# Optimization experiments

Measured on AMD Instinct MI355X. Metric: run time of the kernel, lower is better.

## Reference

```python
import jax, jax.numpy as jnp
import numpy as np
import math

B, N, D, K, H = 64, 16384, 64, 8, 128
ITERS = 3
LN_EPS = 1e-5  # torch LayerNorm default


def _ln(x, w, b):
    m = jnp.mean(x, axis=-1, keepdims=True)
    v = jnp.mean((x - m) ** 2, axis=-1, keepdims=True)
    return (x - m) * jax.lax.rsqrt(v + LN_EPS) * w + b


def setup_inputs() -> dict:
    key = jax.random.key(0)
    ks = jax.random.split(key, 20)
    s = 1.0 / math.sqrt(D)
    inp = {
        "inputs": jax.random.normal(ks[0], (B, N, D), jnp.float32),
        "noise": jax.random.normal(ks[1], (B, K, D), jnp.float32),
        "slots_mu": jax.random.normal(ks[2], (1, 1, D), jnp.float32),
        "slots_sigma": jax.random.uniform(ks[3], (1, 1, D), jnp.float32, -s, s),
        "ln_in_w": jnp.ones((D,), jnp.float32), "ln_in_b": jnp.zeros((D,), jnp.float32),
        "ln_slots_w": jnp.ones((D,), jnp.float32), "ln_slots_b": jnp.zeros((D,), jnp.float32),
        "ln_ff_w": jnp.ones((D,), jnp.float32), "ln_ff_b": jnp.zeros((D,), jnp.float32),
        "wk": jax.random.uniform(ks[4], (D, D), jnp.float32, -s, s),
        "bk": jax.random.uniform(ks[5], (D,), jnp.float32, -s, s),
        "wq": jax.random.uniform(ks[6], (D, D), jnp.float32, -s, s),
        "bq": jax.random.uniform(ks[7], (D,), jnp.float32, -s, s),
        "wv": jax.random.uniform(ks[8], (D, D), jnp.float32, -s, s),
        "bv": jax.random.uniform(ks[9], (D,), jnp.float32, -s, s),
        "gru_wih": jax.random.uniform(ks[10], (D, 3 * D), jnp.float32, -s, s),
        "gru_bih": jax.random.uniform(ks[11], (3 * D,), jnp.float32, -s, s),
        "gru_whh": jax.random.uniform(ks[12], (D, 3 * D), jnp.float32, -s, s),
        "gru_bhh": jax.random.uniform(ks[13], (3 * D,), jnp.float32, -s, s),
        "mlp_w1": jax.random.uniform(ks[14], (D, H), jnp.float32, -s, s),
        "mlp_b1": jax.random.uniform(ks[15], (H,), jnp.float32, -s, s),
        "mlp_w2": jax.random.uniform(ks[16], (H, D), jnp.float32, -1.0 / math.sqrt(H), 1.0 / math.sqrt(H)),
        "mlp_b2": jax.random.uniform(ks[17], (D,), jnp.float32, -1.0 / math.sqrt(H), 1.0 / math.sqrt(H)),
    }
    return inp


def reference(inputs, noise, slots_mu, slots_sigma, ln_in_w, ln_in_b,
              ln_slots_w, ln_slots_b, ln_ff_w, ln_ff_b,
              wk, bk, wq, bq, wv, bv,
              gru_wih, gru_bih, gru_whh, gru_bhh,
              mlp_w1, mlp_b1, mlp_w2, mlp_b2):
    x = _ln(inputs, ln_in_w, ln_in_b)              # [B, N, D]
    # k, v depend only on (fixed) inputs; original recomputes them each iter
    # with identical values, so hoist for efficiency (same math).
    k = x @ wk + bk                                 # [B, N, D]
    v = x @ wv + bv                                 # [B, N, D]
    slots = slots_mu + slots_sigma * noise          # [B, K, D]
    scale = 1.0 / math.sqrt(D)
    for _ in range(ITERS):
        prev = slots
        q = _ln(slots, ln_slots_w, ln_slots_b) @ wq + bq          # [B, K, D]
        logits = jnp.einsum('bkd,bnd->bkn', q, k) * scale          # [B, K, N]
        attn = jax.nn.softmax(logits, axis=1)  # softmax over slots
        updates = jnp.einsum('bkn,bnd->bkd', attn, v)              # [B, K, D]
        # torch GRUCell: gates ordered (r, z, n)
        gi = updates @ gru_wih + gru_bih                           # [B, K, 3D]
        gh = prev @ gru_whh + gru_bhh
        i_r, i_z, i_n = jnp.split(gi, 3, axis=-1)
        h_r, h_z, h_n = jnp.split(gh, 3, axis=-1)
        r = jax.nn.sigmoid(i_r + h_r)
        z = jax.nn.sigmoid(i_z + h_z)
        n = jnp.tanh(i_n + r * h_n)
        slots = (1.0 - z) * n + z * prev
        h = _ln(slots, ln_ff_w, ln_ff_b)
        slots = slots + (jax.nn.relu(h @ mlp_w1 + mlp_b1) @ mlp_w2 + mlp_b2)
    return slots
```

## Files before the change

kernel.cpp:

```cpp
#include <hip/hip_runtime.h>
#include <math.h>

#define B_ 64
#define N_ 16384
#define D_ 64
#define K_ 8
#define SCALE 0.125f
#define LN_EPS 1e-5f
#define CHUNKS 16
#define ROWS_PER_CHUNK (N_ / CHUNKS)
#define NT 256
#define TILES (ROWS_PER_CHUNK / NT)
#define REC 528

__device__ __forceinline__ float wsum64(float v) {
#pragma unroll
  for (int m = 1; m < 64; m <<= 1) v += __shfl_xor(v, m);
  return v;
}

__global__ void init_slots(const float* __restrict__ noise, const float* __restrict__ mu,
                           const float* __restrict__ sg, float* __restrict__ slots) {
  int i = blockIdx.x * blockDim.x + threadIdx.x;
  int d = i & 63;
  slots[i] = mu[d] + sg[d] * noise[i];
}

__global__ __launch_bounds__(64) void prep_q(
    const float* __restrict__ slots,
    const float* __restrict__ lnsw, const float* __restrict__ lnsb,
    const float* __restrict__ wq, const float* __restrict__ bq,
    const float* __restrict__ wk, const float* __restrict__ bk,
    const float* __restrict__ lniw, const float* __restrict__ lnib,
    float* __restrict__ qprep) {
  const int bk_i = blockIdx.x;
  const int b = bk_i >> 3, kk = bk_i & 7;
  const int d = threadIdx.x;
  __shared__ float xs[64], qsh[64], wkl[64 * 65];
  for (int i = 0; i < 64; ++i) wkl[i * 65 + d] = wk[i * 64 + d];
  float s = slots[bk_i * 64 + d];
  float m = wsum64(s) * (1.f / 64.f);
  float df = s - m;
  float var = wsum64(df * df) * (1.f / 64.f);
  float r = 1.f / sqrtf(var + LN_EPS);
  xs[d] = df * r * lnsw[d] + lnsb[d];
  __syncthreads();
  float q = bq[d];
  for (int c = 0; c < 64; ++c) q += xs[c] * wq[c * 64 + d];
  qsh[d] = q;
  __syncthreads();
  float qp = 0.f, c0 = 0.f;
  for (int dd = 0; dd < 64; ++dd) {
    float qd = qsh[dd];
    qp += wkl[d * 65 + dd] * qd;
    c0 += qd * bk[dd];
  }
  float qw = qp * lniw[d] * SCALE;
  float As = wsum64(qw);
  float Bp = wsum64(qp * lnib[d]);
  float Bc = (Bp + c0) * SCALE;
  float* rec = qprep + b * REC;
  rec[d * 8 + kk] = qw;
  if (d == 0) { rec[512 + kk] = As; rec[520 + kk] = Bc; }
}

__global__ __launch_bounds__(256) void attn_pass(
    const float* __restrict__ inp, const float* __restrict__ qprep,
    float* __restrict__ part) {
  __shared__ float xT[64 * 129];
  __shared__ float awr[4 * 512];
  __shared__ float qwT[512];
  __shared__ float AsBc[16];
  __shared__ float redS[4 * 16];
  __shared__ float accST[16];
  const int tid = threadIdx.x;
  const int b = blockIdx.x >> 4, chunk = blockIdx.x & 15;
  for (int i = tid; i < 512; i += 256) qwT[i] = qprep[b * REC + i];
  if (tid < 16) { AsBc[tid] = qprep[b * REC + 512 + tid]; accST[tid] = 0.f; }
  __syncthreads();
  const int kk0 = (tid >> 6) * 2;
  const int dd = tid & 63;
  float Y0 = 0.f, Y1 = 0.f;
  const float* srcbase = inp + ((size_t)b * N_ + (size_t)chunk * ROWS_PER_CHUNK) * D_;
  for (int t = 0; t < TILES; ++t) {
    const float* src = srcbase + (size_t)(t * NT + tid) * D_;
    float4 x[16];
#pragma unroll
    for (int j = 0; j < 16; ++j) x[j] = reinterpret_cast<const float4*>(src)[j];
    float sum = 0.f, sq = 0.f;
    float l[8];
#pragma unroll
    for (int kk = 0; kk < 8; ++kk) l[kk] = 0.f;
#pragma unroll
    for (int j = 0; j < 16; ++j) {
      float xc[4] = {x[j].x, x[j].y, x[j].z, x[j].w};
#pragma unroll
      for (int e = 0; e < 4; ++e) {
        const int c = j * 4 + e;
        const float v = xc[e];
        sum += v; sq += v * v;
        const float4 qa = *reinterpret_cast<const float4*>(&qwT[c * 8]);
        const float4 qb = *reinterpret_cast<const float4*>(&qwT[c * 8 + 4]);
        l[0] += qa.x * v; l[1] += qa.y * v; l[2] += qa.z * v; l[3] += qa.w * v;
        l[4] += qb.x * v; l[5] += qb.y * v; l[6] += qb.z * v; l[7] += qb.w * v;
      }
    }
    const float m = sum * (1.f / 64.f);
    const float var = sq * (1.f / 64.f) - m * m;
    const float r = 1.f / sqrtf(var + LN_EPS);
    const float mr = m * r;
    float lmax = -1e30f;
#pragma unroll
    for (int kk = 0; kk < 8; ++kk) {
      l[kk] = r * l[kk] - mr * AsBc[kk] + AsBc[8 + kk];
      lmax = fmaxf(lmax, l[kk]);
    }
    float es = 0.f;
#pragma unroll
    for (int kk = 0; kk < 8; ++kk) { l[kk] = expf(l[kk] - lmax); es += l[kk]; }
    const float inv = 1.f / es;
#pragma unroll
    for (int kk = 0; kk < 8; ++kk) l[kk] *= inv;
#pragma unroll
    for (int p = 0; p < 4; ++p) {
      float2 w2; w2.x = l[2 * p] * r; w2.y = l[2 * p + 1] * r;
      *reinterpret_cast<float2*>(&awr[p * 512 + tid * 2]) = w2;
    }
    float red[16];
#pragma unroll
    for (int kk = 0; kk < 8; ++kk) {
      red[kk] = wsum64(l[kk]);
      red[8 + kk] = wsum64(l[kk] * mr);
    }
    if ((tid & 63) == 0) {
      const int w = tid >> 6;
#pragma unroll
      for (int i = 0; i < 16; ++i) redS[w * 16 + i] = red[i];
    }
    __syncthreads();
    if (tid < 16) accST[tid] += redS[tid] + redS[16 + tid] + redS[32 + tid] + redS[48 + tid];
    if (tid < 128) {
#pragma unroll
      for (int j = 0; j < 16; ++j) {
        xT[(j * 4 + 0) * 129 + tid] = x[j].x;
        xT[(j * 4 + 1) * 129 + tid] = x[j].y;
        xT[(j * 4 + 2) * 129 + tid] = x[j].z;
        xT[(j * 4 + 3) * 129 + tid] = x[j].w;
      }
    }
    __syncthreads();
#pragma unroll 8
    for (int n = 0; n < 128; ++n) {
      const float2 aw = *reinterpret_cast<const float2*>(&awr[(kk0 >> 1) * 512 + n * 2]);
      const float xv = xT[dd * 129 + n];
      Y0 += aw.x * xv; Y1 += aw.y * xv;
    }
    __syncthreads();
    if (tid >= 128) {
      const int tn = tid - 128;
#pragma unroll
      for (int j = 0; j < 16; ++j) {
        xT[(j * 4 + 0) * 129 + tn] = x[j].x;
        xT[(j * 4 + 1) * 129 + tn] = x[j].y;
        xT[(j * 4 + 2) * 129 + tn] = x[j].z;
        xT[(j * 4 + 3) * 129 + tn] = x[j].w;
      }
    }
    __syncthreads();
#pragma unroll 8
    for (int n = 0; n < 128; ++n) {
      const float2 aw = *reinterpret_cast<const float2*>(&awr[(kk0 >> 1) * 512 + (128 + n) * 2]);
      const float xv = xT[dd * 129 + n];
      Y0 += aw.x * xv; Y1 += aw.y * xv;
    }
    __syncthreads();
  }
  float* dst = part + (size_t)blockIdx.x * REC;
  dst[kk0 * 64 + dd] = Y0;
  dst[(kk0 + 1) * 64 + dd] = Y1;
  if (tid < 16) dst[512 + tid] = accST[tid];
}

__global__ __launch_bounds__(64) void gru_mlp(
    const float* __restrict__ part, const float* __restrict__ slots_in,
    const float* __restrict__ lniw, const float* __restrict__ lnib,
    const float* __restrict__ wv, const float* __restrict__ bv,
    const float* __restrict__ wih, const float* __restrict__ bih,
    const float* __restrict__ whh, const float* __restrict__ bhh,
    const float* __restrict__ lnfw, const float* __restrict__ lnfb,
    const float* __restrict__ w1, const float* __restrict__ b1,
    const float* __restrict__ w2, const float* __restrict__ b2,
    float* __restrict__ slots_out) {
  const int bk_i = blockIdx.x;
  const int b = bk_i >> 3, kk = bk_i & 7;
  const int d = threadIdx.x;
  __shared__ float xs[64], ush[64], psh[64], hsh[64], hid[128];
  float Y = 0.f, S = 0.f, T1 = 0.f;
  for (int ch = 0; ch < 16; ++ch) {
    const float* p = part + (size_t)(b * 16 + ch) * REC;
    Y += p[kk * 64 + d];
    S += p[512 + kk];
    T1 += p[520 + kk];
  }
  xs[d] = lniw[d] * (Y - T1) + lnib[d] * S;
  const float prev = slots_in[bk_i * 64 + d];
  psh[d] = prev;
  __syncthreads();
  float u = S * bv[d];
  for (int c = 0; c < 64; ++c) u += wv[c * 64 + d] * xs[c];
  ush[d] = u;
  __syncthreads();
  float g0 = bih[d], g1 = bih[64 + d], g2 = bih[128 + d];
  float h0 = bhh[d], h1 = bhh[64 + d], h2 = bhh[128 + d];
  for (int c = 0; c < 64; ++c) {
    const float uc = ush[c], pc = psh[c];
    g0 += uc * wih[c * 192 + d];
    g1 += uc * wih[c * 192 + 64 + d];
    g2 += uc * wih[c * 192 + 128 + d];
    h0 += pc * whh[c * 192 + d];
    h1 += pc * whh[c * 192 + 64 + d];
    h2 += pc * whh[c * 192 + 128 + d];
  }
  const float r = 1.f / (1.f + expf(-(g0 + h0)));
  const float z = 1.f / (1.f + expf(-(g1 + h1)));
  const float nn = tanhf(g2 + r * h2);
  const float sn = (1.f - z) * nn + z * prev;
  const float m = wsum64(sn) * (1.f / 64.f);
  const float df = sn - m;
  const float var = wsum64(df * df) * (1.f / 64.f);
  const float rr = 1.f / sqrtf(var + LN_EPS);
  const float h = df * rr * lnfw[d] + lnfb[d];
  hsh[d] = h;
  __syncthreads();
  float a0 = b1[d], a1 = b1[64 + d];
  for (int c = 0; c < 64; ++c) {
    const float hc = hsh[c];
    a0 += hc * w1[c * 128 + d];
    a1 += hc * w1[c * 128 + 64 + d];
  }
  hid[d] = fmaxf(a0, 0.f);
  hid[64 + d] = fmaxf(a1, 0.f);
  __syncthreads();
  float o = b2[d];
  for (int j = 0; j < 128; ++j) o += hid[j] * w2[j * 64 + d];
  slots_out[bk_i * 64 + d] = sn + o;
}

extern "C" void kernel_launch(void* const* d_in, const int* in_sizes, int n_in,
                              void* d_out, int out_size, void* d_ws, size_t ws_size,
                              hipStream_t stream) {
  const float* inp   = (const float*)d_in[0];
  const float* noise = (const float*)d_in[1];
  const float* mu    = (const float*)d_in[2];
  const float* sg    = (const float*)d_in[3];
  const float* lniw  = (const float*)d_in[4];
  const float* lnib  = (const float*)d_in[5];
  const float* lnsw  = (const float*)d_in[6];
  const float* lnsb  = (const float*)d_in[7];
  const float* lnfw  = (const float*)d_in[8];
  const float* lnfb  = (const float*)d_in[9];
  const float* wk    = (const float*)d_in[10];
  const float* bk    = (const float*)d_in[11];
  const float* wq    = (const float*)d_in[12];
  const float* bq    = (const float*)d_in[13];
  const float* wv    = (const float*)d_in[14];
  const float* bv    = (const float*)d_in[15];
  const float* wih   = (const float*)d_in[16];
  const float* bih   = (const float*)d_in[17];
  const float* whh   = (const float*)d_in[18];
  const float* bhh   = (const float*)d_in[19];
  const float* w1    = (const float*)d_in[20];
  const float* b1    = (const float*)d_in[21];
  const float* w2    = (const float*)d_in[22];
  const float* b2    = (const float*)d_in[23];
  float* ws = (float*)d_ws;
  float* slots = ws;
  float* qprep = ws + 32768;
  float* part  = ws + 32768 + 64 * REC;
  float* out   = (float*)d_out;
  init_slots<<<64, 512, 0, stream>>>(noise, mu, sg, slots);
  for (int it = 0; it < 3; ++it) {
    prep_q<<<B_ * K_, 64, 0, stream>>>(slots, lnsw, lnsb, wq, bq, wk, bk, lniw, lnib, qprep);
    attn_pass<<<B_ * CHUNKS, 256, 0, stream>>>(inp, qprep, part);
    gru_mlp<<<B_ * K_, 64, 0, stream>>>(part, slots, lniw, lnib, wv, bv, wih, bih, whh, bhh,
                                        lnfw, lnfb, w1, b1, w2, b2, (it == 2) ? out : slots);
  }
}
```

Baseline: 363.9 us.

## Restructure attention pass with register prefetch and fuse q-prep into slot update

The attention kernel now uses 8 chunks per batch instead of 16, prefetches the next tile of inputs into registers while the current tile is processed, and stores rows to a swizzled row-major LDS layout. Each thread accumulates a 2x4 block of the weighted sum with float4 reads, and the softmax statistics are reduced once at the end instead of every tile. The GRU/MLP kernel is widened to 256 threads that split the matvecs over input channels, and it also computes the next iteration's q preparation, which removes two prep_q launches. This adds register pressure and halves the grid size, leaving 512 blocks on the GPU.

```diff
diff --git a/kernel.cpp b/kernel.cpp
--- a/kernel.cpp
+++ b/kernel.cpp
@@ -7,10 +7,9 @@
 #define K_ 8
 #define SCALE 0.125f
 #define LN_EPS 1e-5f
-#define CHUNKS 16
+#define CHUNKS 8
 #define ROWS_PER_CHUNK (N_ / CHUNKS)
-#define NT 256
-#define TILES (ROWS_PER_CHUNK / NT)
+#define TILES (ROWS_PER_CHUNK / 256)
 #define REC 528
 
 __device__ __forceinline__ float wsum64(float v) {
@@ -64,33 +63,29 @@
   if (d == 0) { rec[512 + kk] = As; rec[520 + kk] = Bc; }
 }
 
-__global__ __launch_bounds__(256) void attn_pass(
+__global__ __launch_bounds__(256, 2) void attn_pass(
     const float* __restrict__ inp, const float* __restrict__ qprep,
     float* __restrict__ part) {
-  __shared__ float xT[64 * 129];
-  __shared__ float awr[4 * 512];
-  __shared__ float qwT[512];
-  __shared__ float AsBc[16];
-  __shared__ float redS[4 * 16];
-  __shared__ float accST[16];
+  __shared__ __align__(16) float xrow[256 * 68];
+  __shared__ float2 aw[4 * 257];
+  __shared__ float redST[64];
   const int tid = threadIdx.x;
-  const int b = blockIdx.x >> 4, chunk = blockIdx.x & 15;
-  for (int i = tid; i < 512; i += 256) qwT[i] = qprep[b * REC + i];
-  if (tid < 16) { AsBc[tid] = qprep[b * REC + 512 + tid]; accST[tid] = 0.f; }
-  __syncthreads();
-  const int kk0 = (tid >> 6) * 2;
-  const int dd = tid & 63;
-  float Y0 = 0.f, Y1 = 0.f;
+  const int b = blockIdx.x >> 3, chunk = blockIdx.x & 7;
+  const int p = tid & 3, dq = (tid >> 2) & 15, w = tid >> 6;
+  const float* __restrict__ qp = qprep + b * REC;
   const float* srcbase = inp + ((size_t)b * N_ + (size_t)chunk * ROWS_PER_CHUNK) * D_;
+  float4 x[16];
+  {
+    const float4* s = reinterpret_cast<const float4*>(srcbase + (size_t)tid * D_);
+#pragma unroll
+    for (int j = 0; j < 16; ++j) x[j] = s[j];
+  }
+  float Ya[8] = {0.f, 0.f, 0.f, 0.f, 0.f, 0.f, 0.f, 0.f};
+  float sS[8] = {0.f, 0.f, 0.f, 0.f, 0.f, 0.f, 0.f, 0.f};
+  float sT[8] = {0.f, 0.f, 0.f, 0.f, 0.f, 0.f, 0.f, 0.f};
   for (int t = 0; t < TILES; ++t) {
-    const float* src = srcbase + (size_t)(t * NT + tid) * D_;
-    float4 x[16];
-#pragma unroll
-    for (int j = 0; j < 16; ++j) x[j] = reinterpret_cast<const float4*>(src)[j];
     float sum = 0.f, sq = 0.f;
-    float l[8];
-#pragma unroll
-    for (int kk = 0; kk < 8; ++kk) l[kk] = 0.f;
+    float l[8] = {0.f, 0.f, 0.f, 0.f, 0.f, 0.f, 0.f, 0.f};
 #pragma unroll
     for (int j = 0; j < 16; ++j) {
       float xc[4] = {x[j].x, x[j].y, x[j].z, x[j].w};
@@ -99,10 +94,8 @@
         const int c = j * 4 + e;
         const float v = xc[e];
         sum += v; sq += v * v;
-        const float4 qa = *reinterpret_cast<const float4*>(&qwT[c * 8]);
-        const float4 qb = *reinterpret_cast<const float4*>(&qwT[c * 8 + 4]);
-        l[0] += qa.x * v; l[1] += qa.y * v; l[2] += qa.z * v; l[3] += qa.w * v;
-        l[4] += qb.x * v; l[5] += qb.y * v; l[6] += qb.z * v; l[7] += qb.w * v;
+#pragma unroll
+        for (int kq = 0; kq < 8; ++kq) l[kq] += qp[c * 8 + kq] * v;
       }
     }
     const float m = sum * (1.f / 64.f);
@@ -111,78 +104,77 @@
     const float mr = m * r;
     float lmax = -1e30f;
 #pragma unroll
-    for (int kk = 0; kk < 8; ++kk) {
-      l[kk] = r * l[kk] - mr * AsBc[kk] + AsBc[8 + kk];
-      lmax = fmaxf(lmax, l[kk]);
+    for (int kq = 0; kq < 8; ++kq) {
+      l[kq] = r * l[kq] - mr * qp[512 + kq] + qp[520 + kq];
+      lmax = fmaxf(lmax, l[kq]);
     }
     float es = 0.f;
 #pragma unroll
-    for (int kk = 0; kk < 8; ++kk) { l[kk] = expf(l[kk] - lmax); es += l[kk]; }
+    for (int kq = 0; kq < 8; ++kq) { l[kq] = __expf(l[kq] - lmax); es += l[kq]; }
     const float inv = 1.f / es;
 #pragma unroll
-    for (int kk = 0; kk < 8; ++kk) l[kk] *= inv;
-#pragma unroll
-    for (int p = 0; p < 4; ++p) {
-      float2 w2; w2.x = l[2 * p] * r; w2.y = l[2 * p + 1] * r;
-      *reinterpret_cast<float2*>(&awr[p * 512 + tid * 2]) = w2;
-    }
-    float red[16];
-#pragma unroll
-    for (int kk = 0; kk < 8; ++kk) {
-      red[kk] = wsum64(l[kk]);
-      red[8 + kk] = wsum64(l[kk] * mr);
-    }
-    if ((tid & 63) == 0) {
-      const int w = tid >> 6;
-#pragma unroll
-      for (int i = 0; i < 16; ++i) redS[w * 16 + i] = red[i];
+    for (int kq = 0; kq < 8; ++kq) {
+      l[kq] *= inv;
+      sS[kq] += l[kq];
+      sT[kq] += l[kq] * mr;
+    }
+#pragma unroll
+    for (int pp = 0; pp < 4; ++pp) {
+      float2 v2; v2.x = l[2 * pp] * r; v2.y = l[2 * pp + 1] * r;
+      aw[pp * 257 + tid] = v2;
+    }
+    {
+      float* dst = &xrow[tid * 68];
+      const int rs = tid >> 3;
+#pragma unroll
+      for (int j = 0; j < 16; ++j) {
+        const int cs = (j + rs) & 15;
+        *reinterpret_cast<float4*>(dst + cs * 4) = x[j];
+      }
+    }
+    if (t + 1 < TILES) {
+      const float4* s = reinterpret_cast<const float4*>(srcbase + (size_t)((t + 1) * 256 + tid) * D_);
+#pragma unroll
+      for (int j = 0; j < 16; ++j) x[j] = s[j];
     }
     __syncthreads();
-    if (tid < 16) accST[tid] += redS[tid] + redS[16 + tid] + redS[32 + tid] + redS[48 + tid];
-    if (tid < 128) {
-#pragma unroll
-      for (int j = 0; j < 16; ++j) {
-        xT[(j * 4 + 0) * 129 + tid] = x[j].x;
-        xT[(j * 4 + 1) * 129 + tid] = x[j].y;
-        xT[(j * 4 + 2) * 129 + tid] = x[j].z;
-        xT[(j * 4 + 3) * 129 + tid] = x[j].w;
-      }
+#pragma unroll 4
+    for (int i = 0; i < 64; ++i) {
+      const int nl = w * 64 + i;
+      const float2 a2 = aw[p * 257 + nl];
+      const float4 xv = *reinterpret_cast<const float4*>(
+          &xrow[nl * 68 + (((dq + (nl >> 3)) & 15) << 2)]);
+      Ya[0] += a2.x * xv.x; Ya[1] += a2.x * xv.y; Ya[2] += a2.x * xv.z; Ya[3] += a2.x * xv.w;
+      Ya[4] += a2.y * xv.x; Ya[5] += a2.y * xv.y; Ya[6] += a2.y * xv.z; Ya[7] += a2.y * xv.w;
     }
     __syncthreads();
-#pragma unroll 8
-    for (int n = 0; n < 128; ++n) {
-      const float2 aw = *reinterpret_cast<const float2*>(&awr[(kk0 >> 1) * 512 + n * 2]);
-      const float xv = xT[dd * 129 + n];
-      Y0 += aw.x * xv; Y1 += aw.y * xv;
-    }
-    __syncthreads();
-    if (tid >= 128) {
-      const int tn = tid - 128;
-#pragma unroll
-      for (int j = 0; j < 16; ++j) {
-        xT[(j * 4 + 0) * 129 + tn] = x[j].x;
-        xT[(j * 4 + 1) * 129 + tn] = x[j].y;
-        xT[(j * 4 + 2) * 129 + tn] = x[j].z;
-        xT[(j * 4 + 3) * 129 + tn] = x[j].w;
-      }
-    }
-    __syncthreads();
-#pragma unroll 8
-    for (int n = 0; n < 128; ++n) {
-      const float2 aw = *reinterpret_cast<const float2*>(&awr[(kk0 >> 1) * 512 + (128 + n) * 2]);
-      const float xv = xT[dd * 129 + n];
-      Y0 += aw.x * xv; Y1 += aw.y * xv;
-    }
-    __syncthreads();
-  }
+  }
+#pragma unroll
+  for (int kq = 0; kq < 8; ++kq) { sS[kq] = wsum64(sS[kq]); sT[kq] = wsum64(sT[kq]); }
+  if ((tid & 63) == 0) {
+#pragma unroll
+    for (int i = 0; i < 8; ++i) { redST[w * 16 + i] = sS[i]; redST[w * 16 + 8 + i] = sT[i]; }
+  }
+  float* yred = xrow;
+  *reinterpret_cast<float4*>(&yred[tid * 12]) = make_float4(Ya[0], Ya[1], Ya[2], Ya[3]);
+  *reinterpret_cast<float4*>(&yred[tid * 12 + 4]) = make_float4(Ya[4], Ya[5], Ya[6], Ya[7]);
+  __syncthreads();
   float* dst = part + (size_t)blockIdx.x * REC;
-  dst[kk0 * 64 + dd] = Y0;
-  dst[(kk0 + 1) * 64 + dd] = Y1;
-  if (tid < 16) dst[512 + tid] = accST[tid];
-}
-
-__global__ __launch_bounds__(64) void gru_mlp(
-    const float* __restrict__ part, const float* __restrict__ slots_in,
+  for (int o = tid; o < 512; o += 256) {
+    const int kq = o >> 6, dd = o & 63;
+    const int pp = kq >> 1, kkl = kq & 1, dqq = dd >> 2, jj = dd & 3;
+    float v = 0.f;
+#pragma unroll
+    for (int ww = 0; ww < 4; ++ww)
+      v += yred[(ww * 64 + dqq * 4 + pp) * 12 + kkl * 4 + jj];
+    dst[o] = v;
+  }
+  if (tid < 16)
+    dst[512 + tid] = redST[tid] + redST[16 + tid] + redST[32 + tid] + redST[48 + tid];
+}
+
+__global__ __launch_bounds__(256) void slot_update(
+    const float* __restrict__ part, const float* slots_in,
     const float* __restrict__ lniw, const float* __restrict__ lnib,
     const float* __restrict__ wv, const float* __restrict__ bv,
     const float* __restrict__ wih, const float* __restrict__ bih,
@@ -190,60 +182,138 @@
     const float* __restrict__ lnfw, const float* __restrict__ lnfb,
     const float* __restrict__ w1, const float* __restrict__ b1,
     const float* __restrict__ w2, const float* __restrict__ b2,
-    float* __restrict__ slots_out) {
-  const int bk_i = blockIdx.x;
-  const int b = bk_i >> 3, kk = bk_i & 7;
-  const int d = threadIdx.x;
-  __shared__ float xs[64], ush[64], psh[64], hsh[64], hid[128];
-  float Y = 0.f, S = 0.f, T1 = 0.f;
-  for (int ch = 0; ch < 16; ++ch) {
-    const float* p = part + (size_t)(b * 16 + ch) * REC;
-    Y += p[kk * 64 + d];
-    S += p[512 + kk];
-    T1 += p[520 + kk];
-  }
-  xs[d] = lniw[d] * (Y - T1) + lnib[d] * S;
+    const float* __restrict__ lnsw, const float* __restrict__ lnsb,
+    const float* __restrict__ wq, const float* __restrict__ bq,
+    const float* __restrict__ wk, const float* __restrict__ bkv,
+    float* slots_out, float* __restrict__ qprep, const int do_prep) {
+  const int bk_i = blockIdx.x, b = bk_i >> 3, kk = bk_i & 7;
+  const int tid = threadIdx.x, cq = tid >> 6, d = tid & 63;
+  const int c0 = cq * 16;
+  __shared__ float pA[4][68], pB[4][68], pC[4][68], pD[4][68];
+  __shared__ float xsh[64], psh[64], ush[64], hsh[64], snsh[64], qsh[64];
+  __shared__ float hid1[2][132];
+  const float* pb = part + (size_t)(b * CHUNKS) * REC;
+  float S = 0.f, T1 = 0.f;
+#pragma unroll
+  for (int ch = 0; ch < CHUNKS; ++ch) {
+    S += pb[ch * REC + 512 + kk];
+    T1 += pb[ch * REC + 520 + kk];
+  }
+  float y = 0.f;
+#pragma unroll
+  for (int cc = 0; cc < 2; ++cc)
+    y += pb[(cq * 2 + cc) * REC + kk * 64 + d];
+  pA[cq][d] = y;
   const float prev = slots_in[bk_i * 64 + d];
-  psh[d] = prev;
-  __syncthreads();
-  float u = S * bv[d];
-  for (int c = 0; c < 64; ++c) u += wv[c * 64 + d] * xs[c];
-  ush[d] = u;
-  __syncthreads();
-  float g0 = bih[d], g1 = bih[64 + d], g2 = bih[128 + d];
-  float h0 = bhh[d], h1 = bhh[64 + d], h2 = bhh[128 + d];
-  for (int c = 0; c < 64; ++c) {
-    const float uc = ush[c], pc = psh[c];
-    g0 += uc * wih[c * 192 + d];
-    g1 += uc * wih[c * 192 + 64 + d];
-    g2 += uc * wih[c * 192 + 128 + d];
-    h0 += pc * whh[c * 192 + d];
-    h1 += pc * whh[c * 192 + 64 + d];
-    h2 += pc * whh[c * 192 + 128 + d];
-  }
-  const float r = 1.f / (1.f + expf(-(g0 + h0)));
-  const float z = 1.f / (1.f + expf(-(g1 + h1)));
-  const float nn = tanhf(g2 + r * h2);
-  const float sn = (1.f - z) * nn + z * prev;
-  const float m = wsum64(sn) * (1.f / 64.f);
-  const float df = sn - m;
-  const float var = wsum64(df * df) * (1.f / 64.f);
-  const float rr = 1.f / sqrtf(var + LN_EPS);
-  const float h = df * rr * lnfw[d] + lnfb[d];
-  hsh[d] = h;
-  __syncthreads();
-  float a0 = b1[d], a1 = b1[64 + d];
-  for (int c = 0; c < 64; ++c) {
-    const float hc = hsh[c];
-    a0 += hc * w1[c * 128 + d];
-    a1 += hc * w1[c * 128 + 64 + d];
-  }
-  hid[d] = fmaxf(a0, 0.f);
-  hid[64 + d] = fmaxf(a1, 0.f);
-  __syncthreads();
-  float o = b2[d];
-  for (int j = 0; j < 128; ++j) o += hid[j] * w2[j * 64 + d];
-  slots_out[bk_i * 64 + d] = sn + o;
+  if (cq == 0) psh[d] = prev;
+  __syncthreads();
+  if (cq == 0) {
+    const float Y = pA[0][d] + pA[1][d] + pA[2][d] + pA[3][d];
+    xsh[d] = lniw[d] * (Y - T1) + lnib[d] * S;
+  }
+  __syncthreads();
+  {
+    float up = 0.f, h0 = 0.f, h1 = 0.f, h2 = 0.f;
+    for (int c = c0; c < c0 + 16; ++c) {
+      const float xc = xsh[c], pc = psh[c];
+      up += wv[c * 64 + d] * xc;
+      h0 += pc * whh[c * 192 + d];
+      h1 += pc * whh[c * 192 + 64 + d];
+      h2 += pc * whh[c * 192 + 128 + d];
+    }
+    pA[cq][d] = up; pB[cq][d] = h0; pC[cq][d] = h1; pD[cq][d] = h2;
+  }
+  __syncthreads();
+  float hh0 = 0.f, hh1 = 0.f, hh2 = 0.f;
+  if (cq == 0) {
+    ush[d] = S * bv[d] + pA[0][d] + pA[1][d] + pA[2][d] + pA[3][d];
+    hh0 = bhh[d] + pB[0][d] + pB[1][d] + pB[2][d] + pB[3][d];
+    hh1 = bhh[64 + d] + pC[0][d] + pC[1][d] + pC[2][d] + pC[3][d];
+    hh2 = bhh[128 + d] + pD[0][d] + pD[1][d] + pD[2][d] + pD[3][d];
+  }
+  __syncthreads();
+  {
+    float g0 = 0.f, g1 = 0.f, g2 = 0.f;
+    for (int c = c0; c < c0 + 16; ++c) {
+      const float uc = ush[c];
+      g0 += uc * wih[c * 192 + d];
+      g1 += uc * wih[c * 192 + 64 + d];
+      g2 += uc * wih[c * 192 + 128 + d];
+    }
+    pA[cq][d] = g0; pB[cq][d] = g1; pC[cq][d] = g2;
+  }
+  __syncthreads();
+  if (cq == 0) {
+    const float gi0 = bih[d] + pA[0][d] + pA[1][d] + pA[2][d] + pA[3][d];
+    const float gi1 = bih[64 + d] + pB[0][d] + pB[1][d] + pB[2][d] + pB[3][d];
+    const float gi2 = bih[128 + d] + pC[0][d] + pC[1][d] + pC[2][d] + pC[3][d];
+    const float rg = 1.f / (1.f + __expf(-(gi0 + hh0)));
+    const float zg = 1.f / (1.f + __expf(-(gi1 + hh1)));
+    const float ng = tanhf(gi2 + rg * hh2);
+    const float sn = (1.f - zg) * ng + zg * prev;
+    const float mm = wsum64(sn) * (1.f / 64.f);
+    const float df = sn - mm;
+    const float vv = wsum64(df * df) * (1.f / 64.f);
+    const float rr = 1.f / sqrtf(vv + LN_EPS);
+    snsh[d] = sn;
+    hsh[d] = df * rr * lnfw[d] + lnfb[d];
+  }
+  __syncthreads();
+  {
+    const int j = tid & 127, ch2 = tid >> 7;
+    float a = 0.f;
+    for (int c = ch2 * 32; c < ch2 * 32 + 32; ++c) a += hsh[c] * w1[c * 128 + j];
+    hid1[ch2][j] = a;
+  }
+  __syncthreads();
+  {
+    float o = 0.f;
+    for (int j2 = cq * 32; j2 < cq * 32 + 32; ++j2) {
+      const float hv = fmaxf(hid1[0][j2] + hid1[1][j2] + b1[j2], 0.f);
+      o += hv * w2[j2 * 64 + d];
+    }
+    pA[cq][d] = o;
+  }
+  __syncthreads();
+  float news = 0.f;
+  if (cq == 0) {
+    news = snsh[d] + b2[d] + pA[0][d] + pA[1][d] + pA[2][d] + pA[3][d];
+    slots_out[bk_i * 64 + d] = news;
+  }
+  if (!do_prep) return;
+  if (cq == 0) {
+    const float mm = wsum64(news) * (1.f / 64.f);
+    const float df = news - mm;
+    const float vv = wsum64(df * df) * (1.f / 64.f);
+    const float rr = 1.f / sqrtf(vv + LN_EPS);
+    xsh[d] = df * rr * lnsw[d] + lnsb[d];
+  }
+  __syncthreads();
+  {
+    float qpt = 0.f;
+    for (int c = c0; c < c0 + 16; ++c) qpt += xsh[c] * wq[c * 64 + d];
+    pB[cq][d] = qpt;
+  }
+  __syncthreads();
+  if (cq == 0) qsh[d] = bq[d] + pB[0][d] + pB[1][d] + pB[2][d] + pB[3][d];
+  __syncthreads();
+  {
+    float qq = 0.f;
+    for (int dd2 = c0; dd2 < c0 + 16; ++dd2) qq += wk[d * 64 + dd2] * qsh[dd2];
+    pC[cq][d] = qq;
+  }
+  __syncthreads();
+  if (cq == 0) {
+    const float qpv = pC[0][d] + pC[1][d] + pC[2][d] + pC[3][d];
+    const float c0v = wsum64(qsh[d] * bkv[d]);
+    const float qw = qpv * lniw[d] * SCALE;
+    const float As = wsum64(qw);
+    const float Bp = wsum64(qpv * lnib[d]);
+    const float Bc = (Bp + c0v) * SCALE;
+    float* rec = qprep + b * REC;
+    rec[d * 8 + kk] = qw;
+    if (d == 0) { rec[512 + kk] = As; rec[520 + kk] = Bc; }
+  }
 }
 
 extern "C" void kernel_launch(void* const* d_in, const int* in_sizes, int n_in,
@@ -279,10 +349,12 @@
   float* part  = ws + 32768 + 64 * REC;
   float* out   = (float*)d_out;
   init_slots<<<64, 512, 0, stream>>>(noise, mu, sg, slots);
+  prep_q<<<B_ * K_, 64, 0, stream>>>(slots, lnsw, lnsb, wq, bq, wk, bk, lniw, lnib, qprep);
   for (int it = 0; it < 3; ++it) {
-    prep_q<<<B_ * K_, 64, 0, stream>>>(slots, lnsw, lnsb, wq, bq, wk, bk, lniw, lnib, qprep);
     attn_pass<<<B_ * CHUNKS, 256, 0, stream>>>(inp, qprep, part);
-    gru_mlp<<<B_ * K_, 64, 0, stream>>>(part, slots, lniw, lnib, wv, bv, wih, bih, whh, bhh,
-                                        lnfw, lnfb, w1, b1, w2, b2, (it == 2) ? out : slots);
-  }
-}
+    slot_update<<<B_ * K_, 256, 0, stream>>>(
+        part, slots, lniw, lnib, wv, bv, wih, bih, whh, bhh,
+        lnfw, lnfb, w1, b1, w2, b2, lnsw, lnsb, wq, bq, wk, bk,
+        (it == 2) ? out : slots, qprep, (it < 2) ? 1 : 0);
+  }
+}
```

Measured after the change: 376.2 us. 1.03x slower.
